# Performance work log

Measured on AMD Instinct MI355X. Metric: run time of the kernel, lower is better.

Reference implementation:

```python
import jax, jax.numpy as jnp
import numpy as np

N_U = 50000
N_V = 50000
N = N_U + N_V
DEG = 16                      # avg degree per user on bipartite graph
E_UND = N_U * DEG             # undirected edges
D_IN = 128
D_OUT = 128


def setup_inputs() -> dict:
    key = jax.random.key(0)
    k1, k2, k3, k4, k5, k6 = jax.random.split(key, 6)
    u_f = jax.random.normal(k1, (N_U, D_IN), dtype=jnp.float32)
    v_f = jax.random.normal(k2, (N_V, D_IN), dtype=jnp.float32)
    # xavier-uniform-like init for projection weights
    lim = float(np.sqrt(6.0 / (D_IN + D_OUT)))
    u_w = jax.random.uniform(k3, (D_IN, D_OUT), minval=-lim, maxval=lim, dtype=jnp.float32)
    v_w = jax.random.uniform(k4, (D_IN, D_OUT), minval=-lim, maxval=lim, dtype=jnp.float32)
    # bipartite edges: user u -- item (N_U + v); DGL graph stores both directions
    u_idx = jax.random.randint(k5, (E_UND,), 0, N_U, dtype=jnp.int32)
    v_idx = jax.random.randint(k6, (E_UND,), 0, N_V, dtype=jnp.int32) + N_U
    src = jnp.concatenate([u_idx, v_idx])  # [E]
    dst = jnp.concatenate([v_idx, u_idx])  # [E]
    return {"u_f": u_f, "v_f": v_f, "u_w": u_w, "v_w": v_w, "src": src, "dst": dst}


def reference(u_f, v_f, u_w, v_w, src, dst):
    # optional per-side projection (weight=True)
    node_f = jnp.concatenate([u_f @ u_w, v_f @ v_w], axis=0)          # [N, D_OUT]
    ones = jnp.ones(src.shape[0], dtype=node_f.dtype)
    deg_out = jnp.clip(jax.ops.segment_sum(ones, src, num_segments=N), 1.0)  # out-degrees
    node_f = node_f * (deg_out ** -0.5)[:, None]
    # update_all(copy_u, sum): gather by src, segment-sum by dst
    rst = jax.ops.segment_sum(node_f[src], dst, num_segments=N)       # [N, D_OUT]
    deg_in = jnp.clip(jax.ops.segment_sum(ones, dst, num_segments=N), 1.0)   # in-degrees
    rst = rst * (deg_in ** -0.5)[:, None]
    return rst  # activation is None
```

## Files before the change

kernel.cpp:

```cpp
#include <hip/hip_runtime.h>

#define D 128
#define TN_PROJ 64
#define MAXDEG 64
#define NPART 8
#define NSLICE 256

typedef __attribute__((ext_vector_type(8))) short short8;
typedef __attribute__((ext_vector_type(4))) float f32x4;

__device__ __forceinline__ unsigned short f2bf(float x) {
    union { float f; unsigned u; } c; c.f = x;
    unsigned r = c.u + 0x7FFFu + ((c.u >> 16) & 1u);
    return (unsigned short)(r >> 16);
}
__device__ __forceinline__ float blo(unsigned u) {
    union { unsigned u; float f; } c; c.u = u << 16; return c.f;
}
__device__ __forceinline__ float bhi(unsigned u) {
    union { unsigned u; float f; } c; c.u = u & 0xFFFF0000u; return c.f;
}

__global__ __launch_bounds__(256) void wprep_kernel(
    const float* __restrict__ u_w, const float* __restrict__ v_w,
    unsigned short* __restrict__ wt)
{
    int idx = blockIdx.x * 256 + threadIdx.x;
    int side = idx >> 14;
    int r = idx & 16383;
    int k = r >> 7, col = r & 127;
    const float* w = side ? v_w : u_w;
    wt[(size_t)side * 16384 + (size_t)col * 128 + k] = f2bf(w[(size_t)k * 128 + col]);
}

__global__ __launch_bounds__(256) void fill_kernel(
    const int* __restrict__ src, const int* __restrict__ dst,
    int* __restrict__ deg, unsigned short* __restrict__ adj,
    int n_u, int n, int n_und)
{
    const int part  = blockIdx.x & (NPART - 1);
    const int slice = blockIdx.x / NPART;
    const int psize = (n + NPART - 1) / NPART;
    const int lo = part * psize;
    const int hi = min(n, lo + psize);
    const int chunk = (n_und + NSLICE - 1) / NSLICE;
    const int beg = slice * chunk;
    const int end = min(n_und, beg + chunk);

    for (int e = beg + threadIdx.x; e < end; e += 256) {
        int u = src[e];
        int v = dst[e];
        if (v >= lo && v < hi) {
            int p = atomicAdd(&deg[v], 1);
            if (p < MAXDEG) adj[(size_t)v * MAXDEG + p] = (unsigned short)u;
        }
        if (u >= lo && u < hi) {
            int p = atomicAdd(&deg[u], 1);
            if (p < MAXDEG) adj[(size_t)u * MAXDEG + p] = (unsigned short)(v - n_u);
        }
    }
}

__global__ __launch_bounds__(256) void proj_kernel(
    const float* __restrict__ f,
    const unsigned short* __restrict__ wt,
    const int* __restrict__ deg,
    unsigned short* __restrict__ nf,
    int n)
{
    __shared__ unsigned short alds[TN_PROJ * D];
    __shared__ unsigned short blds[D * D];
    const int t = threadIdx.x;
    const int base = blockIdx.x * TN_PROJ;

    #pragma unroll
    for (int c = 0; c < 8; ++c) {
        int lin = (t + c * 256) * 16;
        int row = lin >> 8;
        int dsto = lin ^ ((row & 7) << 4);
        uint4 val = *(const uint4*)((const char*)wt + lin);
        *(uint4*)((char*)blds + dsto) = val;
    }
    {
        int r = t >> 2;
        int kq = (t & 3) * 32;
        int gn = base + r;
        #pragma unroll
        for (int c = 0; c < 4; ++c) {
            int k = kq + c * 8;
            float4 x0 = make_float4(0.f, 0.f, 0.f, 0.f), x1 = x0;
            if (gn < n) {
                x0 = *(const float4*)&f[(size_t)gn * D + k];
                x1 = *(const float4*)&f[(size_t)gn * D + k + 4];
            }
            ushort4 p0, p1;
            p0.x = f2bf(x0.x); p0.y = f2bf(x0.y); p0.z = f2bf(x0.z); p0.w = f2bf(x0.w);
            p1.x = f2bf(x1.x); p1.y = f2bf(x1.y); p1.z = f2bf(x1.z); p1.w = f2bf(x1.w);
            uint4 packed;
            packed.x = (unsigned)p0.x | ((unsigned)p0.y << 16);
            packed.y = (unsigned)p0.z | ((unsigned)p0.w << 16);
            packed.z = (unsigned)p1.x | ((unsigned)p1.y << 16);
            packed.w = (unsigned)p1.z | ((unsigned)p1.w << 16);
            int byte = r * 256 + k * 2;
            int dsto = byte ^ ((r & 7) << 4);
            *(uint4*)((char*)alds + dsto) = packed;
        }
    }
    __syncthreads();

    const int wv = t >> 6;
    const int lane = t & 63;
    const int cb = wv * 32;
    const int lrow = lane & 15;
    const int lk = (lane >> 4) * 8;

    f32x4 acc[4][2] = {};

    #pragma unroll
    for (int ks = 0; ks < 4; ++ks) {
        int k2 = (ks * 32 + lk) * 2;
        int br0 = cb + lrow, br1 = cb + 16 + lrow;
        short8 b0 = *(const short8*)((const char*)blds + ((br0 * 256 + k2) ^ ((br0 & 7) << 4)));
        short8 b1 = *(const short8*)((const char*)blds + ((br1 * 256 + k2) ^ ((br1 & 7) << 4)));
        #pragma unroll
        for (int nt = 0; nt < 4; ++nt) {
            int ar = 16 * nt + lrow;
            short8 a = *(const short8*)((const char*)alds + ((ar * 256 + k2) ^ ((ar & 7) << 4)));
            acc[nt][0] = __builtin_amdgcn_mfma_f32_16x16x32_bf16(a, b0, acc[nt][0], 0, 0, 0);
            acc[nt][1] = __builtin_amdgcn_mfma_f32_16x16x32_bf16(a, b1, acc[nt][1], 0, 0, 0);
        }
    }

    #pragma unroll
    for (int nt = 0; nt < 4; ++nt) {
        #pragma unroll
        for (int rr = 0; rr < 4; ++rr) {
            int node = base + 16 * nt + (lane >> 4) * 4 + rr;
            if (node < n) {
                float sc = rsqrtf((float)max(deg[node], 1));
                #pragma unroll
                for (int ct = 0; ct < 2; ++ct) {
                    int col = cb + 16 * ct + (lane & 15);
                    nf[(size_t)node * D + col] = f2bf(acc[nt][ct][rr] * sc);
                }
            }
        }
    }
}

__global__ __launch_bounds__(256) void gather_kernel(
    const int* __restrict__ deg, const unsigned short* __restrict__ adj,
    const unsigned short* __restrict__ nodef,
    float* __restrict__ out, int n_u, int n)
{
    const int node = (blockIdx.x * 256 + threadIdx.x) >> 4;
    const int l    = threadIdx.x & 15;
    const int gb   = threadIdx.x & 48;
    if (node >= n) return;
    const int dn  = deg[node];
    const int len = min(dn, MAXDEG);
    const int sbase = (node < n_u) ? n_u : 0;
    const unsigned short* row = adj + (size_t)node * MAXDEG;

    float acc[8] = {};

    for (int b = 0; b < len; b += 16) {
        int sreg = (b + l < len) ? (int)row[b + l] : 0;
        int cnt = min(len - b, 16);
        #pragma unroll 4
        for (int j = 0; j < cnt; ++j) {
            int s = __shfl(sreg, gb | j) + sbase;
            uint4 q = *(const uint4*)&nodef[(size_t)s * D + l * 8];
            acc[0] += blo(q.x); acc[1] += bhi(q.x);
            acc[2] += blo(q.y); acc[3] += bhi(q.y);
            acc[4] += blo(q.z); acc[5] += bhi(q.z);
            acc[6] += blo(q.w); acc[7] += bhi(q.w);
        }
    }

    const float sd = rsqrtf((float)max(dn, 1));
    float4 o0 = make_float4(acc[0] * sd, acc[1] * sd, acc[2] * sd, acc[3] * sd);
    float4 o1 = make_float4(acc[4] * sd, acc[5] * sd, acc[6] * sd, acc[7] * sd);
    float* op = &out[(size_t)node * D + l * 8];
    *(float4*)(op)     = o0;
    *(float4*)(op + 4) = o1;
}

extern "C" void kernel_launch(void* const* d_in, const int* in_sizes, int n_in,
                              void* d_out, int out_size, void* d_ws, size_t ws_size,
                              hipStream_t stream) {
    const float* u_f = (const float*)d_in[0];
    const float* v_f = (const float*)d_in[1];
    const float* u_w = (const float*)d_in[2];
    const float* v_w = (const float*)d_in[3];
    const int*   src = (const int*)d_in[4];
    const int*   dst = (const int*)d_in[5];

    const int n_u = in_sizes[0] / D;
    const int n_v = in_sizes[1] / D;
    const int n   = n_u + n_v;
    const int n_e = in_sizes[4];
    const int n_und = n_e / 2;
    float* out = (float*)d_out;

    char* ws = (char*)d_ws;
    size_t off = 0;
    unsigned short* nodef = (unsigned short*)(ws + off); off += (size_t)n * D * sizeof(unsigned short);
    int* deg = (int*)(ws + off); off += (size_t)n * sizeof(int);
    unsigned short* adj = (unsigned short*)(ws + off); off += (size_t)n * MAXDEG * sizeof(unsigned short);
    unsigned short* wt = (unsigned short*)(ws + off); off += (size_t)2 * 128 * 128 * sizeof(unsigned short);

    hipMemsetAsync(deg, 0, (size_t)n * sizeof(int), stream);

    wprep_kernel<<<128, 256, 0, stream>>>(u_w, v_w, wt);

    fill_kernel<<<NPART * NSLICE, 256, 0, stream>>>(src, dst, deg, adj, n_u, n, n_und);

    const int nbu = (n_u + TN_PROJ - 1) / TN_PROJ;
    proj_kernel<<<nbu, 256, 0, stream>>>(u_f, wt, deg, nodef, n_u);
    const int nbv = (n_v + TN_PROJ - 1) / TN_PROJ;
    proj_kernel<<<nbv, 256, 0, stream>>>(v_f, wt + 16384, deg + n_u,
                                         nodef + (size_t)n_u * D, n_v);

    const int nb_g = (n * 16 + 255) / 256;
    gather_kernel<<<nb_g, 256, 0, stream>>>(deg, adj, nodef, out, n_u, n);
}
```

Baseline: 176.7 us.

## Fuse adjacency fill and projection into one launch, move source-degree scaling to gather

The edge fill and both projection GEMMs now run in one kernel launch, with blocks split by index. This lets the atomic-bound fill overlap the MFMA projection. The projection no longer depends on degrees: the source-degree rsqrt scaling moves into the gather, where each neighbor's scale is loaded and shuffled alongside its index. The projection also drops LDS staging and reads A from global memory and B from the global weight copy directly in registers. In exchange the gather does extra random degree reads and multiplies per edge, and B is re-read from global/L2 by every wave.

```diff
diff --git a/kernel.cpp b/kernel.cpp
--- a/kernel.cpp
+++ b/kernel.cpp
@@ -1,7 +1,6 @@
 #include <hip/hip_runtime.h>
 
 #define D 128
-#define TN_PROJ 64
 #define MAXDEG 64
 #define NPART 8
 #define NSLICE 256
@@ -33,116 +32,84 @@
     wt[(size_t)side * 16384 + (size_t)col * 128 + k] = f2bf(w[(size_t)k * 128 + col]);
 }
 
-__global__ __launch_bounds__(256) void fill_kernel(
+__global__ __launch_bounds__(256) void fused_kernel(
     const int* __restrict__ src, const int* __restrict__ dst,
     int* __restrict__ deg, unsigned short* __restrict__ adj,
-    int n_u, int n, int n_und)
+    const float* __restrict__ u_f, const float* __restrict__ v_f,
+    const unsigned short* __restrict__ wt,
+    unsigned short* __restrict__ nodef,
+    int n_u, int n_v, int n, int n_und)
 {
-    const int part  = blockIdx.x & (NPART - 1);
-    const int slice = blockIdx.x / NPART;
-    const int psize = (n + NPART - 1) / NPART;
-    const int lo = part * psize;
-    const int hi = min(n, lo + psize);
-    const int chunk = (n_und + NSLICE - 1) / NSLICE;
-    const int beg = slice * chunk;
-    const int end = min(n_und, beg + chunk);
+    const int F = NPART * NSLICE;
+    if ((int)blockIdx.x < F) {
+        const int part  = blockIdx.x & (NPART - 1);
+        const int slice = blockIdx.x / NPART;
+        const int psize = (n + NPART - 1) / NPART;
+        const int lo = part * psize;
+        const int hi = min(n, lo + psize);
+        const int chunk = (n_und + NSLICE - 1) / NSLICE;
+        const int beg = slice * chunk;
+        const int end = min(n_und, beg + chunk);
 
-    for (int e = beg + threadIdx.x; e < end; e += 256) {
-        int u = src[e];
-        int v = dst[e];
-        if (v >= lo && v < hi) {
-            int p = atomicAdd(&deg[v], 1);
-            if (p < MAXDEG) adj[(size_t)v * MAXDEG + p] = (unsigned short)u;
+        for (int e = beg + threadIdx.x; e < end; e += 256) {
+            int u = src[e];
+            int v = dst[e];
+            if (v >= lo && v < hi) {
+                int p = atomicAdd(&deg[v], 1);
+                if (p < MAXDEG) adj[(size_t)v * MAXDEG + p] = (unsigned short)u;
+            }
+            if (u >= lo && u < hi) {
+                int p = atomicAdd(&deg[u], 1);
+                if (p < MAXDEG) adj[(size_t)u * MAXDEG + p] = (unsigned short)(v - n_u);
+            }
         }
-        if (u >= lo && u < hi) {
-            int p = atomicAdd(&deg[u], 1);
-            if (p < MAXDEG) adj[(size_t)u * MAXDEG + p] = (unsigned short)(v - n_u);
-        }
+        return;
     }
-}
 
-__global__ __launch_bounds__(256) void proj_kernel(
-    const float* __restrict__ f,
-    const unsigned short* __restrict__ wt,
-    const int* __restrict__ deg,
-    unsigned short* __restrict__ nf,
-    int n)
-{
-    __shared__ unsigned short alds[TN_PROJ * D];
-    __shared__ unsigned short blds[D * D];
-    const int t = threadIdx.x;
-    const int base = blockIdx.x * TN_PROJ;
+    const int pb  = blockIdx.x - F;
+    const int nbu = (n_u + 63) >> 6;
+    const float* f; const unsigned short* w; unsigned short* nf; int ns; int base;
+    if (pb < nbu) { f = u_f; w = wt;         nf = nodef;                   ns = n_u; base = pb * 64; }
+    else          { f = v_f; w = wt + 16384; nf = nodef + (size_t)n_u * D; ns = n_v; base = (pb - nbu) * 64; }
+
+    const int lane = threadIdx.x & 63;
+    const int wv   = threadIdx.x >> 6;
+    const int lrow = lane & 15;
+    const int lk   = (lane >> 4) * 8;
+    const int arow = base + wv * 16 + lrow;
+    const bool av  = arow < ns;
+    const size_t abase = (size_t)arow * D;
 
     #pragma unroll
-    for (int c = 0; c < 8; ++c) {
-        int lin = (t + c * 256) * 16;
-        int row = lin >> 8;
-        int dsto = lin ^ ((row & 7) << 4);
-        uint4 val = *(const uint4*)((const char*)wt + lin);
-        *(uint4*)((char*)blds + dsto) = val;
-    }
-    {
-        int r = t >> 2;
-        int kq = (t & 3) * 32;
-        int gn = base + r;
+    for (int ch = 0; ch < 2; ++ch) {
+        f32x4 acc[4] = {};
         #pragma unroll
-        for (int c = 0; c < 4; ++c) {
-            int k = kq + c * 8;
-            float4 x0 = make_float4(0.f, 0.f, 0.f, 0.f), x1 = x0;
-            if (gn < n) {
-                x0 = *(const float4*)&f[(size_t)gn * D + k];
-                x1 = *(const float4*)&f[(size_t)gn * D + k + 4];
+        for (int ks = 0; ks < 4; ++ks) {
+            const int k = ks * 32 + lk;
+            short8 a = {};
+            if (av) {
+                float4 x0 = *(const float4*)&f[abase + k];
+                float4 x1 = *(const float4*)&f[abase + k + 4];
+                a[0] = (short)f2bf(x0.x); a[1] = (short)f2bf(x0.y);
+                a[2] = (short)f2bf(x0.z); a[3] = (short)f2bf(x0.w);
+                a[4] = (short)f2bf(x1.x); a[5] = (short)f2bf(x1.y);
+                a[6] = (short)f2bf(x1.z); a[7] = (short)f2bf(x1.w);
             }
-            ushort4 p0, p1;
-            p0.x = f2bf(x0.x); p0.y = f2bf(x0.y); p0.z = f2bf(x0.z); p0.w = f2bf(x0.w);
-            p1.x = f2bf(x1.x); p1.y = f2bf(x1.y); p1.z = f2bf(x1.z); p1.w = f2bf(x1.w);
-            uint4 packed;
-            packed.x = (unsigned)p0.x | ((unsigned)p0.y << 16);
-            packed.y = (unsigned)p0.z | ((unsigned)p0.w << 16);
-            packed.z = (unsigned)p1.x | ((unsigned)p1.y << 16);
-            packed.w = (unsigned)p1.z | ((unsigned)p1.w << 16);
-            int byte = r * 256 + k * 2;
-            int dsto = byte ^ ((r & 7) << 4);
-            *(uint4*)((char*)alds + dsto) = packed;
+            #pragma unroll
+            for (int ct = 0; ct < 4; ++ct) {
+                const int col16 = ch * 4 + ct;
+                short8 b = *(const short8*)&w[(size_t)(col16 * 16 + lrow) * D + k];
+                acc[ct] = __builtin_amdgcn_mfma_f32_16x16x32_bf16(a, b, acc[ct], 0, 0, 0);
+            }
         }
-    }
-    __syncthreads();
-
-    const int wv = t >> 6;
-    const int lane = t & 63;
-    const int cb = wv * 32;
-    const int lrow = lane & 15;
-    const int lk = (lane >> 4) * 8;
-
-    f32x4 acc[4][2] = {};
-
-    #pragma unroll
-    for (int ks = 0; ks < 4; ++ks) {
-        int k2 = (ks * 32 + lk) * 2;
-        int br0 = cb + lrow, br1 = cb + 16 + lrow;
-        short8 b0 = *(const short8*)((const char*)blds + ((br0 * 256 + k2) ^ ((br0 & 7) << 4)));
-        short8 b1 = *(const short8*)((const char*)blds + ((br1 * 256 + k2) ^ ((br1 & 7) << 4)));
+        const int crow = base + wv * 16 + (lane >> 4) * 4;
         #pragma unroll
-        for (int nt = 0; nt < 4; ++nt) {
-            int ar = 16 * nt + lrow;
-            short8 a = *(const short8*)((const char*)alds + ((ar * 256 + k2) ^ ((ar & 7) << 4)));
-            acc[nt][0] = __builtin_amdgcn_mfma_f32_16x16x32_bf16(a, b0, acc[nt][0], 0, 0, 0);
-            acc[nt][1] = __builtin_amdgcn_mfma_f32_16x16x32_bf16(a, b1, acc[nt][1], 0, 0, 0);
-        }
-    }
-
-    #pragma unroll
-    for (int nt = 0; nt < 4; ++nt) {
-        #pragma unroll
-        for (int rr = 0; rr < 4; ++rr) {
-            int node = base + 16 * nt + (lane >> 4) * 4 + rr;
-            if (node < n) {
-                float sc = rsqrtf((float)max(deg[node], 1));
-                #pragma unroll
-                for (int ct = 0; ct < 2; ++ct) {
-                    int col = cb + 16 * ct + (lane & 15);
-                    nf[(size_t)node * D + col] = f2bf(acc[nt][ct][rr] * sc);
-                }
+        for (int ct = 0; ct < 4; ++ct) {
+            const int col = (ch * 4 + ct) * 16 + lrow;
+            #pragma unroll
+            for (int rr = 0; rr < 4; ++rr) {
+                const int node = crow + rr;
+                if (node < ns) nf[(size_t)node * D + col] = f2bf(acc[ct][rr]);
             }
         }
     }
@@ -165,16 +132,22 @@
     float acc[8] = {};
 
     for (int b = 0; b < len; b += 16) {
-        int sreg = (b + l < len) ? (int)row[b + l] : 0;
-        int cnt = min(len - b, 16);
-        #pragma unroll 4
+        const int idx = b + l;
+        int sreg = 0; float screg = 0.f;
+        if (idx < len) {
+            sreg  = (int)row[idx] + sbase;
+            screg = rsqrtf((float)max(deg[sreg], 1));
+        }
+        const int cnt = min(len - b, 16);
+        #pragma unroll 8
         for (int j = 0; j < cnt; ++j) {
-            int s = __shfl(sreg, gb | j) + sbase;
+            const int   s = __shfl(sreg,  gb | j);
+            const float c = __shfl(screg, gb | j);
             uint4 q = *(const uint4*)&nodef[(size_t)s * D + l * 8];
-            acc[0] += blo(q.x); acc[1] += bhi(q.x);
-            acc[2] += blo(q.y); acc[3] += bhi(q.y);
-            acc[4] += blo(q.z); acc[5] += bhi(q.z);
-            acc[6] += blo(q.w); acc[7] += bhi(q.w);
+            acc[0] += c * blo(q.x); acc[1] += c * bhi(q.x);
+            acc[2] += c * blo(q.y); acc[3] += c * bhi(q.y);
+            acc[4] += c * blo(q.z); acc[5] += c * bhi(q.z);
+            acc[6] += c * blo(q.w); acc[7] += c * bhi(q.w);
         }
     }
 
@@ -214,13 +187,11 @@
 
     wprep_kernel<<<128, 256, 0, stream>>>(u_w, v_w, wt);
 
-    fill_kernel<<<NPART * NSLICE, 256, 0, stream>>>(src, dst, deg, adj, n_u, n, n_und);
-
-    const int nbu = (n_u + TN_PROJ - 1) / TN_PROJ;
-    proj_kernel<<<nbu, 256, 0, stream>>>(u_f, wt, deg, nodef, n_u);
-    const int nbv = (n_v + TN_PROJ - 1) / TN_PROJ;
-    proj_kernel<<<nbv, 256, 0, stream>>>(v_f, wt + 16384, deg + n_u,
-                                         nodef + (size_t)n_u * D, n_v);
+    const int F   = NPART * NSLICE;
+    const int nbu = (n_u + 63) >> 6;
+    const int nbv = (n_v + 63) >> 6;
+    fused_kernel<<<F + nbu + nbv, 256, 0, stream>>>(
+        src, dst, deg, adj, u_f, v_f, wt, nodef, n_u, n_v, n, n_und);
 
     const int nb_g = (n * 16 + 255) / 256;
     gather_kernel<<<nb_g, 256, 0, stream>>>(deg, adj, nodef, out, n_u, n);
```

New measurement: 185.4 us. +4.9%, slower.
